# Kernel optimization log

Measured on AMD Instinct MI355X. Metric: run time of the kernel, lower is better.

Reference implementation:

```python
import jax, jax.numpy as jnp
import numpy as np

N_NODES = 50000
D_FEAT = 128
N_EDGES = 500000


def setup_inputs() -> dict:
    key = jax.random.key(0)
    ks = jax.random.split(key, 9)
    scale1 = 1.0 / np.sqrt(2 * D_FEAT)
    scale2 = 1.0 / np.sqrt(512)
    scale3 = 1.0 / np.sqrt(256)
    return {
        "node_features": jax.random.normal(ks[0], (N_NODES, D_FEAT), dtype=jnp.float32),
        "edge_label_index": jax.random.randint(ks[1], (2, N_EDGES), 0, N_NODES, dtype=jnp.int64),
        "W1": jax.random.normal(ks[2], (512, 2 * D_FEAT), dtype=jnp.float32) * scale1,
        "b1": jax.random.normal(ks[3], (512,), dtype=jnp.float32) * scale1,
        "W2": jax.random.normal(ks[4], (256, 512), dtype=jnp.float32) * scale2,
        "b2": jax.random.normal(ks[5], (256,), dtype=jnp.float32) * scale2,
        "W3": jax.random.normal(ks[6], (1, 256), dtype=jnp.float32) * scale3,
        "b3": jax.random.normal(ks[7], (1,), dtype=jnp.float32) * scale3,
    }


def reference(node_features, edge_label_index, W1, b1, W2, b2, W3, b3):
    row = edge_label_index[0]
    col = edge_label_index[1]
    # [E, 2*d] gather + concat
    x = jnp.concatenate([node_features[row], node_features[col]], axis=-1)
    x = jax.nn.relu(x @ W1.T + b1)          # [E, 512]
    x = jax.nn.relu(x @ W2.T + b2)          # [E, 256]
    intermediate_x = x
    logits = x @ W3.T + b3                  # [E, 1]
    return (logits.reshape(-1), intermediate_x)
```

## Files before the change

kernel.cpp:

```cpp
#include <hip/hip_runtime.h>
#include <stdint.h>

#define E_TOT 500000
#define EB 64
#define NBLK ((E_TOT + EB - 1) / EB)
#define SWZ(e) (((e) & 7) << 4)

using u32x4  = __attribute__((ext_vector_type(4))) unsigned int;
using f32x4  = __attribute__((ext_vector_type(4))) float;
using short8 = __attribute__((ext_vector_type(8))) short;

__device__ __forceinline__ uint32_t f2bf(float x) {
    uint32_t u = __builtin_bit_cast(uint32_t, x);
    return (u + 0x7fffu + ((u >> 16) & 1u)) >> 16;
}
__device__ __forceinline__ uint32_t pk2(float a, float b) {
    return f2bf(a) | (f2bf(b) << 16);
}

__global__ void prep_weights(const float* __restrict__ W1, const float* __restrict__ W2,
                             unsigned short* __restrict__ w1b, unsigned short* __restrict__ w2b) {
    int t = blockIdx.x * 256 + threadIdx.x;
    int i = t * 4;
    if (i < 131072) {
        float4 f = *reinterpret_cast<const float4*>(W1 + i);
        uint2 u;
        u.x = pk2(f.x, f.y); u.y = pk2(f.z, f.w);
        *reinterpret_cast<uint2*>(w1b + i) = u;
    } else {
        int j = i - 131072;
        float4 f = *reinterpret_cast<const float4*>(W2 + j);
        uint2 u;
        u.x = pk2(f.x, f.y); u.y = pk2(f.z, f.w);
        *reinterpret_cast<uint2*>(w2b + j) = u;
    }
}

template<bool PREPPED>
__global__ __launch_bounds__(512, 4) void fused_mlp(
    const float* __restrict__ nf,
    const int* __restrict__ eidx,
    const char* __restrict__ w1p,
    const char* __restrict__ w2p,
    const float* __restrict__ b1,
    const float* __restrict__ b2,
    const float* __restrict__ w3,
    const float* __restrict__ b3,
    float* __restrict__ out)
{
    __shared__ __align__(16) char xbuf[32768];
    __shared__ __align__(16) char hbuf[32768];
    __shared__ float logit_part[8][EB];

    const int tid  = threadIdx.x;
    const int lane = tid & 63;
    const int wid  = tid >> 6;
    const int hi   = lane >> 4;
    const int lo   = lane & 15;
    const long long e0 = (long long)blockIdx.x * EB;

    {
        int e    = tid >> 3;
        int side = (tid >> 2) & 1;
        int q    = tid & 3;
        long long eg = e0 + e;
        int idx = 0;
        if (eg < E_TOT) idx = eidx[(size_t)side * E_TOT + (size_t)eg];
        const float4* src = reinterpret_cast<const float4*>(nf + (size_t)idx * 128 + q * 32);
        char* dstrow = xbuf + e * 512;
        const int ob = side * 256 + q * 64;
#pragma unroll
        for (int c = 0; c < 4; ++c) {
            float4 f0 = src[2 * c];
            float4 f1 = src[2 * c + 1];
            u32x4 u;
            u[0] = pk2(f0.x, f0.y); u[1] = pk2(f0.z, f0.w);
            u[2] = pk2(f1.x, f1.y); u[3] = pk2(f1.z, f1.w);
            *reinterpret_cast<u32x4*>(dstrow + ((ob + c * 16) ^ SWZ(e))) = u;
        }
    }
    __syncthreads();

    f32x4 acc2[2][4];
#pragma unroll
    for (int mt = 0; mt < 2; ++mt)
#pragma unroll
        for (int nt = 0; nt < 4; ++nt)
            acc2[mt][nt] = f32x4{0.f, 0.f, 0.f, 0.f};

#pragma unroll
    for (int h = 0; h < 2; ++h) {
        f32x4 acc1[2][4];
#pragma unroll
        for (int mt = 0; mt < 2; ++mt)
#pragma unroll
            for (int nt = 0; nt < 4; ++nt)
                acc1[mt][nt] = f32x4{0.f, 0.f, 0.f, 0.f};

#pragma unroll
        for (int kk = 0; kk < 8; ++kk) {
            short8 a[2], b[4];
            if constexpr (PREPPED) {
#pragma unroll
                for (int mt = 0; mt < 2; ++mt) {
                    const int row = h * 256 + wid * 32 + mt * 16 + lo;
                    a[mt] = *reinterpret_cast<const short8*>(w1p + (size_t)row * 512 + kk * 64 + hi * 16);
                }
            } else {
                const float* W1f = reinterpret_cast<const float*>(w1p);
#pragma unroll
                for (int mt = 0; mt < 2; ++mt) {
                    const int row = h * 256 + wid * 32 + mt * 16 + lo;
                    const float* p = W1f + (size_t)row * 256 + kk * 32 + hi * 8;
                    float4 f0 = *reinterpret_cast<const float4*>(p);
                    float4 f1 = *reinterpret_cast<const float4*>(p + 4);
                    u32x4 u;
                    u[0] = pk2(f0.x, f0.y); u[1] = pk2(f0.z, f0.w);
                    u[2] = pk2(f1.x, f1.y); u[3] = pk2(f1.z, f1.w);
                    a[mt] = __builtin_bit_cast(short8, u);
                }
            }
#pragma unroll
            for (int nt = 0; nt < 4; ++nt) {
                int e = nt * 16 + lo;
                b[nt] = *reinterpret_cast<const short8*>(xbuf + e * 512 + ((kk * 64 + hi * 16) ^ SWZ(e)));
            }
#pragma unroll
            for (int nt = 0; nt < 4; ++nt)
#pragma unroll
                for (int mt = 0; mt < 2; ++mt)
                    acc1[mt][nt] = __builtin_amdgcn_mfma_f32_16x16x32_bf16(a[mt], b[nt], acc1[mt][nt], 0, 0, 0);
        }

#pragma unroll
        for (int mt = 0; mt < 2; ++mt) {
            const float4 bias = *reinterpret_cast<const float4*>(b1 + h * 256 + wid * 32 + mt * 16 + hi * 4);
            const int ob = wid * 64 + mt * 32 + hi * 8;
#pragma unroll
            for (int nt = 0; nt < 4; ++nt) {
                int e = nt * 16 + lo;
                f32x4 v = acc1[mt][nt];
                float r0 = fmaxf(v[0] + bias.x, 0.f);
                float r1 = fmaxf(v[1] + bias.y, 0.f);
                float r2 = fmaxf(v[2] + bias.z, 0.f);
                float r3 = fmaxf(v[3] + bias.w, 0.f);
                uint2 u;
                u.x = pk2(r0, r1); u.y = pk2(r2, r3);
                *reinterpret_cast<uint2*>(hbuf + e * 512 + (ob ^ SWZ(e))) = u;
            }
        }
        __syncthreads();

#pragma unroll
        for (int kk = 0; kk < 8; ++kk) {
            short8 a[2], b[4];
            if constexpr (PREPPED) {
#pragma unroll
                for (int mt = 0; mt < 2; ++mt) {
                    const int row = wid * 32 + mt * 16 + lo;
                    a[mt] = *reinterpret_cast<const short8*>(w2p + (size_t)row * 1024 + h * 512 + kk * 64 + hi * 16);
                }
            } else {
                const float* W2f = reinterpret_cast<const float*>(w2p);
#pragma unroll
                for (int mt = 0; mt < 2; ++mt) {
                    const int row = wid * 32 + mt * 16 + lo;
                    const float* p = W2f + (size_t)row * 512 + h * 256 + kk * 32 + hi * 8;
                    float4 f0 = *reinterpret_cast<const float4*>(p);
                    float4 f1 = *reinterpret_cast<const float4*>(p + 4);
                    u32x4 u;
                    u[0] = pk2(f0.x, f0.y); u[1] = pk2(f0.z, f0.w);
                    u[2] = pk2(f1.x, f1.y); u[3] = pk2(f1.z, f1.w);
                    a[mt] = __builtin_bit_cast(short8, u);
                }
            }
#pragma unroll
            for (int nt = 0; nt < 4; ++nt) {
                int e = nt * 16 + lo;
                b[nt] = *reinterpret_cast<const short8*>(hbuf + e * 512 + ((kk * 64 + hi * 16) ^ SWZ(e)));
            }
#pragma unroll
            for (int nt = 0; nt < 4; ++nt)
#pragma unroll
                for (int mt = 0; mt < 2; ++mt)
                    acc2[mt][nt] = __builtin_amdgcn_mfma_f32_16x16x32_bf16(a[mt], b[nt], acc2[mt][nt], 0, 0, 0);
        }
        if (h == 0) __syncthreads();
    }

    {
        float* inter = out + E_TOT;
        float pls[4] = {0.f, 0.f, 0.f, 0.f};
#pragma unroll
        for (int mt = 0; mt < 2; ++mt) {
            const int m = wid * 32 + mt * 16 + hi * 4;
            const float4 bias = *reinterpret_cast<const float4*>(b2 + m);
            const float4 wv   = *reinterpret_cast<const float4*>(w3 + m);
#pragma unroll
            for (int nt = 0; nt < 4; ++nt) {
                long long eg = e0 + nt * 16 + lo;
                f32x4 v = acc2[mt][nt];
                float4 hh;
                hh.x = fmaxf(v[0] + bias.x, 0.f);
                hh.y = fmaxf(v[1] + bias.y, 0.f);
                hh.z = fmaxf(v[2] + bias.z, 0.f);
                hh.w = fmaxf(v[3] + bias.w, 0.f);
                if (eg < E_TOT)
                    *reinterpret_cast<float4*>(inter + (size_t)eg * 256 + m) = hh;
                pls[nt] += hh.x * wv.x + hh.y * wv.y + hh.z * wv.z + hh.w * wv.w;
            }
        }
#pragma unroll
        for (int nt = 0; nt < 4; ++nt) {
            float p = pls[nt];
            p += __shfl_xor(p, 16);
            p += __shfl_xor(p, 32);
            if (hi == 0) logit_part[wid][nt * 16 + lo] = p;
        }
    }
    __syncthreads();
    if (tid < EB) {
        long long eg = e0 + tid;
        if (eg < E_TOT) {
            float s = b3[0];
#pragma unroll
            for (int w = 0; w < 8; ++w) s += logit_part[w][tid];
            out[eg] = s;
        }
    }
}

extern "C" void kernel_launch(void* const* d_in, const int* in_sizes, int n_in,
                              void* d_out, int out_size, void* d_ws, size_t ws_size,
                              hipStream_t stream) {
    const float* nf   = (const float*)d_in[0];
    const int*   eidx = (const int*)d_in[1];
    const float* W1   = (const float*)d_in[2];
    const float* b1   = (const float*)d_in[3];
    const float* W2   = (const float*)d_in[4];
    const float* b2   = (const float*)d_in[5];
    const float* W3   = (const float*)d_in[6];
    const float* b3   = (const float*)d_in[7];
    float* out = (float*)d_out;

    const size_t need = (size_t)(512 * 256 + 256 * 512) * 2;
    if (ws_size >= need) {
        unsigned short* w1b = (unsigned short*)d_ws;
        unsigned short* w2b = w1b + 512 * 256;
        prep_weights<<<256, 256, 0, stream>>>(W1, W2, w1b, w2b);
        fused_mlp<true><<<NBLK, 512, 0, stream>>>(nf, eidx, (const char*)w1b, (const char*)w2b,
                                                  b1, b2, W3, b3, out);
    } else {
        fused_mlp<false><<<NBLK, 512, 0, stream>>>(nf, eidx, (const char*)W1, (const char*)W2,
                                                   b1, b2, W3, b3, out);
    }
}
```

Measured before the change: 593.2 us.

## Double-buffer weight fragment loads and precompute swizzled LDS addresses in MLP kernel

Restructures the K loop of both GEMM phases into chunks of two k-steps. The global weight fragments for the next chunk are prefetched into alternating register buffers while the current chunk's MFMAs run, which is meant to hide global/L2 load latency behind matrix math. The per-step swizzle arithmetic is replaced by per-lane base pointers computed once, with an XOR-64 toggle, and the two LDS buffers are merged into one array at a fixed offset. MFMA blocks are wrapped in s_setprio. The cost is higher register pressure from the doubled A fragments under a 512x4 launch bound.

```diff
diff --git a/kernel.cpp b/kernel.cpp
--- a/kernel.cpp
+++ b/kernel.cpp
@@ -5,6 +5,7 @@
 #define EB 64
 #define NBLK ((E_TOT + EB - 1) / EB)
 #define SWZ(e) (((e) & 7) << 4)
+#define HOFF 32768
 
 using u32x4  = __attribute__((ext_vector_type(4))) unsigned int;
 using f32x4  = __attribute__((ext_vector_type(4))) float;
@@ -16,6 +17,9 @@
 }
 __device__ __forceinline__ uint32_t pk2(float a, float b) {
     return f2bf(a) | (f2bf(b) << 16);
+}
+__device__ __forceinline__ const char* xor64(const char* p) {
+    return (const char*)((uintptr_t)p ^ 64);
 }
 
 __global__ void prep_weights(const float* __restrict__ W1, const float* __restrict__ W2,
@@ -36,6 +40,41 @@
     }
 }
 
+#define CHUNK(ABASE, MTSTR, LDSOFF, ACC, CUR, NXT, C, LAST)                                  \
+  {                                                                                          \
+    if (!(LAST)) {                                                                           \
+      _Pragma("unroll") for (int kkl = 0; kkl < 2; ++kkl)                                    \
+        _Pragma("unroll") for (int mt = 0; mt < 2; ++mt)                                     \
+          NXT[kkl][mt] = *reinterpret_cast<const short8*>(                                   \
+              (ABASE) + mt * (MTSTR) + (((C) + 1) * 2 + kkl) * 64);                          \
+    }                                                                                        \
+    _Pragma("unroll") for (int kkl = 0; kkl < 2; ++kkl) {                                    \
+      const int kk = (C) * 2 + kkl;                                                          \
+      short8 bfr[4];                                                                         \
+      _Pragma("unroll") for (int nt = 0; nt < 4; ++nt) {                                     \
+        const char* bp = (kk & 1) ? xor64(bx0[nt]) : bx0[nt];                                \
+        bfr[nt] = *reinterpret_cast<const short8*>(bp + (LDSOFF) + (kk >> 1) * 128);         \
+      }                                                                                      \
+      __builtin_amdgcn_s_setprio(1);                                                         \
+      _Pragma("unroll") for (int nt = 0; nt < 4; ++nt)                                       \
+        _Pragma("unroll") for (int mt = 0; mt < 2; ++mt)                                     \
+          ACC[mt][nt] = __builtin_amdgcn_mfma_f32_16x16x32_bf16(                             \
+              CUR[kkl][mt], bfr[nt], ACC[mt][nt], 0, 0, 0);                                  \
+      __builtin_amdgcn_s_setprio(0);                                                         \
+    }                                                                                        \
+  }
+
+#define PHASE(ABASE, MTSTR, LDSOFF, ACC)                                                     \
+  {                                                                                          \
+    _Pragma("unroll") for (int kkl = 0; kkl < 2; ++kkl)                                      \
+      _Pragma("unroll") for (int mt = 0; mt < 2; ++mt)                                       \
+        Aa[kkl][mt] = *reinterpret_cast<const short8*>((ABASE) + mt * (MTSTR) + kkl * 64);   \
+    CHUNK(ABASE, MTSTR, LDSOFF, ACC, Aa, Ab, 0, 0)                                           \
+    CHUNK(ABASE, MTSTR, LDSOFF, ACC, Ab, Aa, 1, 0)                                           \
+    CHUNK(ABASE, MTSTR, LDSOFF, ACC, Aa, Ab, 2, 0)                                           \
+    CHUNK(ABASE, MTSTR, LDSOFF, ACC, Ab, Aa, 3, 1)                                           \
+  }
+
 template<bool PREPPED>
 __global__ __launch_bounds__(512, 4) void fused_mlp(
     const float* __restrict__ nf,
@@ -48,8 +87,7 @@
     const float* __restrict__ b3,
     float* __restrict__ out)
 {
-    __shared__ __align__(16) char xbuf[32768];
-    __shared__ __align__(16) char hbuf[32768];
+    __shared__ __align__(16) char smem[65536];
     __shared__ float logit_part[8][EB];
 
     const int tid  = threadIdx.x;
@@ -67,7 +105,7 @@
         int idx = 0;
         if (eg < E_TOT) idx = eidx[(size_t)side * E_TOT + (size_t)eg];
         const float4* src = reinterpret_cast<const float4*>(nf + (size_t)idx * 128 + q * 32);
-        char* dstrow = xbuf + e * 512;
+        char* dstrow = smem + e * 512;
         const int ob = side * 256 + q * 64;
 #pragma unroll
         for (int c = 0; c < 4; ++c) {
@@ -79,6 +117,16 @@
             *reinterpret_cast<u32x4*>(dstrow + ((ob + c * 16) ^ SWZ(e))) = u;
         }
     }
+
+    const char* bx0[4];
+#pragma unroll
+    for (int nt = 0; nt < 4; ++nt) {
+        int e   = nt * 16 + lo;
+        int low = (hi * 16) ^ ((e & 3) << 4);
+        int s6  = (e >> 2) & 1;
+        bx0[nt] = smem + e * 512 + low + 64 * s6;
+    }
+
     __syncthreads();
 
     f32x4 acc2[2][4];
@@ -88,6 +136,8 @@
         for (int nt = 0; nt < 4; ++nt)
             acc2[mt][nt] = f32x4{0.f, 0.f, 0.f, 0.f};
 
+    short8 Aa[2][2], Ab[2][2];
+
 #pragma unroll
     for (int h = 0; h < 2; ++h) {
         f32x4 acc1[2][4];
@@ -97,17 +147,14 @@
             for (int nt = 0; nt < 4; ++nt)
                 acc1[mt][nt] = f32x4{0.f, 0.f, 0.f, 0.f};
 
-#pragma unroll
-        for (int kk = 0; kk < 8; ++kk) {
-            short8 a[2], b[4];
-            if constexpr (PREPPED) {
-#pragma unroll
-                for (int mt = 0; mt < 2; ++mt) {
-                    const int row = h * 256 + wid * 32 + mt * 16 + lo;
-                    a[mt] = *reinterpret_cast<const short8*>(w1p + (size_t)row * 512 + kk * 64 + hi * 16);
-                }
-            } else {
-                const float* W1f = reinterpret_cast<const float*>(w1p);
+        if constexpr (PREPPED) {
+            const char* a1b = w1p + (size_t)(h * 256 + wid * 32 + lo) * 512 + hi * 16;
+            PHASE(a1b, (16 * 512), 0, acc1)
+        } else {
+            const float* W1f = reinterpret_cast<const float*>(w1p);
+#pragma unroll
+            for (int kk = 0; kk < 8; ++kk) {
+                short8 a[2], b[4];
 #pragma unroll
                 for (int mt = 0; mt < 2; ++mt) {
                     const int row = h * 256 + wid * 32 + mt * 16 + lo;
@@ -119,17 +166,17 @@
                     u[2] = pk2(f1.x, f1.y); u[3] = pk2(f1.z, f1.w);
                     a[mt] = __builtin_bit_cast(short8, u);
                 }
+#pragma unroll
+                for (int nt = 0; nt < 4; ++nt) {
+                    const char* bp = (kk & 1) ? xor64(bx0[nt]) : bx0[nt];
+                    b[nt] = *reinterpret_cast<const short8*>(bp + (kk >> 1) * 128);
+                }
+#pragma unroll
+                for (int nt = 0; nt < 4; ++nt)
+#pragma unroll
+                    for (int mt = 0; mt < 2; ++mt)
+                        acc1[mt][nt] = __builtin_amdgcn_mfma_f32_16x16x32_bf16(a[mt], b[nt], acc1[mt][nt], 0, 0, 0);
             }
-#pragma unroll
-            for (int nt = 0; nt < 4; ++nt) {
-                int e = nt * 16 + lo;
-                b[nt] = *reinterpret_cast<const short8*>(xbuf + e * 512 + ((kk * 64 + hi * 16) ^ SWZ(e)));
-            }
-#pragma unroll
-            for (int nt = 0; nt < 4; ++nt)
-#pragma unroll
-                for (int mt = 0; mt < 2; ++mt)
-                    acc1[mt][nt] = __builtin_amdgcn_mfma_f32_16x16x32_bf16(a[mt], b[nt], acc1[mt][nt], 0, 0, 0);
         }
 
 #pragma unroll
@@ -146,22 +193,19 @@
                 float r3 = fmaxf(v[3] + bias.w, 0.f);
                 uint2 u;
                 u.x = pk2(r0, r1); u.y = pk2(r2, r3);
-                *reinterpret_cast<uint2*>(hbuf + e * 512 + (ob ^ SWZ(e))) = u;
+                *reinterpret_cast<uint2*>(smem + HOFF + e * 512 + (ob ^ SWZ(e))) = u;
             }
         }
         __syncthreads();
 
-#pragma unroll
-        for (int kk = 0; kk < 8; ++kk) {
-            short8 a[2], b[4];
-            if constexpr (PREPPED) {
-#pragma unroll
-                for (int mt = 0; mt < 2; ++mt) {
-                    const int row = wid * 32 + mt * 16 + lo;
-                    a[mt] = *reinterpret_cast<const short8*>(w2p + (size_t)row * 1024 + h * 512 + kk * 64 + hi * 16);
-                }
-            } else {
-                const float* W2f = reinterpret_cast<const float*>(w2p);
+        if constexpr (PREPPED) {
+            const char* a2b = w2p + (size_t)(wid * 32 + lo) * 1024 + h * 512 + hi * 16;
+            PHASE(a2b, (16 * 1024), HOFF, acc2)
+        } else {
+            const float* W2f = reinterpret_cast<const float*>(w2p);
+#pragma unroll
+            for (int kk = 0; kk < 8; ++kk) {
+                short8 a[2], b[4];
 #pragma unroll
                 for (int mt = 0; mt < 2; ++mt) {
                     const int row = wid * 32 + mt * 16 + lo;
@@ -173,17 +217,17 @@
                     u[2] = pk2(f1.x, f1.y); u[3] = pk2(f1.z, f1.w);
                     a[mt] = __builtin_bit_cast(short8, u);
                 }
+#pragma unroll
+                for (int nt = 0; nt < 4; ++nt) {
+                    const char* bp = (kk & 1) ? xor64(bx0[nt]) : bx0[nt];
+                    b[nt] = *reinterpret_cast<const short8*>(bp + HOFF + (kk >> 1) * 128);
+                }
+#pragma unroll
+                for (int nt = 0; nt < 4; ++nt)
+#pragma unroll
+                    for (int mt = 0; mt < 2; ++mt)
+                        acc2[mt][nt] = __builtin_amdgcn_mfma_f32_16x16x32_bf16(a[mt], b[nt], acc2[mt][nt], 0, 0, 0);
             }
-#pragma unroll
-            for (int nt = 0; nt < 4; ++nt) {
-                int e = nt * 16 + lo;
-                b[nt] = *reinterpret_cast<const short8*>(hbuf + e * 512 + ((kk * 64 + hi * 16) ^ SWZ(e)));
-            }
-#pragma unroll
-            for (int nt = 0; nt < 4; ++nt)
-#pragma unroll
-                for (int mt = 0; mt < 2; ++mt)
-                    acc2[mt][nt] = __builtin_amdgcn_mfma_f32_16x16x32_bf16(a[mt], b[nt], acc2[mt][nt], 0, 0, 0);
         }
         if (h == 0) __syncthreads();
     }
```

After: 730.7 us. 1.23x slower.
